# Kernel optimization log

Measured on AMD Instinct MI355X. Metric: run time of the kernel, lower is better.

## Reference

```python
import jax, jax.numpy as jnp
import numpy as np

N_NODES = 100000
N_EDGES = 1600000
N_GRAPHS = 256
D_IN = 128
D_HID = 128
D_OUT = 64


def graph_conv(x, src, dst, W_rel, b_rel, W_root):
    # PyG GraphConv: out = lin_rel(mean_{j->i} x_j) + lin_root(x)
    msgs = jax.ops.segment_sum(x[src], dst, num_segments=N_NODES)  # [N, d]
    deg = jax.ops.segment_sum(jnp.ones((src.shape[0],), x.dtype), dst, num_segments=N_NODES)
    agg = msgs / jnp.maximum(deg, 1.0)[:, None]
    return agg @ W_rel + b_rel + x @ W_root


def setup_inputs() -> dict:
    key = jax.random.key(0)
    ks = jax.random.split(key, 12)
    x = jax.random.normal(ks[0], (N_NODES, D_IN), dtype=jnp.float32)
    edge_index = jax.random.randint(ks[1], (2, N_EDGES), 0, N_NODES, dtype=jnp.int64)
    batch = jnp.sort(jax.random.randint(ks[2], (N_NODES,), 0, N_GRAPHS, dtype=jnp.int64))
    def lin(k, fan_in, fan_out):
        bound = 1.0 / np.sqrt(fan_in)
        return jax.random.uniform(k, (fan_in, fan_out), jnp.float32, -bound, bound)
    inp = {
        "x": x, "edge_index": edge_index, "batch": batch,
        "W1_rel": lin(ks[3], D_IN, D_HID), "b1_rel": jnp.zeros((D_HID,), jnp.float32), "W1_root": lin(ks[4], D_IN, D_HID),
        "W2_rel": lin(ks[5], D_HID, D_HID), "b2_rel": jnp.zeros((D_HID,), jnp.float32), "W2_root": lin(ks[6], D_HID, D_HID),
        "W3_rel": lin(ks[7], D_HID, D_HID), "b3_rel": jnp.zeros((D_HID,), jnp.float32), "W3_root": lin(ks[8], D_HID, D_HID),
        "Wl": lin(ks[9], D_HID, D_OUT), "bl": jnp.zeros((D_OUT,), jnp.float32),
    }
    return inp


def reference(x, edge_index, batch, W1_rel, b1_rel, W1_root, W2_rel, b2_rel, W2_root,
              W3_rel, b3_rel, W3_root, Wl, bl):
    src, dst = edge_index[0], edge_index[1]
    h = jax.nn.relu(graph_conv(x, src, dst, W1_rel, b1_rel, W1_root))
    h = jax.nn.relu(graph_conv(h, src, dst, W2_rel, b2_rel, W2_root))
    h = graph_conv(h, src, dst, W3_rel, b3_rel, W3_root)
    # global mean pool over graphs
    sums = jax.ops.segment_sum(h, batch, num_segments=N_GRAPHS)          # [G, d]
    cnts = jax.ops.segment_sum(jnp.ones((h.shape[0],), h.dtype), batch, num_segments=N_GRAPHS)
    pooled = sums / jnp.maximum(cnts, 1.0)[:, None]
    # dropout is identity at inference
    return pooled @ Wl + bl  # [G, D_OUT]
```

## Files before the change

### kernel.cpp

```cpp
#include <hip/hip_runtime.h>
#include <hip/hip_bf16.h>

#define N_NODES  100000
#define N_EDGES  1600000
#define N_GRAPHS 256
#define DCH      128
#define DOUT     64
#define NB       391
#define PADB     512
#define SLACK    4608
#define CHUNK    4096
#define PCH      64

typedef short v8s __attribute__((ext_vector_type(8)));
typedef float v4f __attribute__((ext_vector_type(4)));

static __device__ __forceinline__ float bf2f(unsigned short u) {
    unsigned int x = ((unsigned int)u) << 16;
    return __builtin_bit_cast(float, x);
}
static __device__ __forceinline__ unsigned short f2bf(float f) {
    unsigned int x = __builtin_bit_cast(unsigned int, f);
    unsigned int r = (x + 0x7fffu + ((x >> 16) & 1u)) >> 16;
    return (unsigned short)r;
}
static __device__ __forceinline__ int clampi(int v, int lo, int hi) {
    return v < lo ? lo : (v > hi ? hi : v);
}

__global__ void cvt_kernel(const float* __restrict__ in, unsigned short* __restrict__ out) {
    size_t i = ((size_t)blockIdx.x * blockDim.x + threadIdx.x) * 4;
    if (i + 3 < (size_t)N_NODES * DCH) {
        float4 f = *reinterpret_cast<const float4*>(in + i);
        uint2 o;
        o.x = ((unsigned)f2bf(f.y) << 16) | (unsigned)f2bf(f.x);
        o.y = ((unsigned)f2bf(f.w) << 16) | (unsigned)f2bf(f.z);
        *reinterpret_cast<uint2*>(out + i) = o;
    }
}

__global__ void __launch_bounds__(256) binA_kernel(const int* __restrict__ src, const int* __restrict__ dst,
                                                   int* __restrict__ gcur, uint2* __restrict__ region) {
    __shared__ uint2 stage[CHUNK];
    __shared__ int hcnt[PADB], hcnt2[PADB], hoff[PADB], garr[PADB];
    __shared__ int s2[256];
    int tid = threadIdx.x;
    int e0  = blockIdx.x * CHUNK;
    int nedge = N_EDGES - e0; if (nedge > CHUNK) nedge = CHUNK;

    for (int b = tid; b < PADB; b += 256) { hcnt[b] = 0; hcnt2[b] = 0; }
    __syncthreads();

    int es[16], ed[16];
    #pragma unroll
    for (int j = 0; j < 16; j++) {
        int e = e0 + j * 256 + tid;
        if (e < N_EDGES) {
            es[j] = clampi(src[e], 0, N_NODES - 1);
            ed[j] = clampi(dst[e], 0, N_NODES - 1);
            atomicAdd(&hcnt[ed[j] >> 8], 1);
        } else { es[j] = -1; ed[j] = 0; }
    }
    __syncthreads();

    int v0 = hcnt[2 * tid], v1 = hcnt[2 * tid + 1];
    s2[tid] = v0 + v1; __syncthreads();
    for (int off = 1; off < 256; off <<= 1) {
        int x = (tid >= off) ? s2[tid - off] : 0;
        __syncthreads();
        s2[tid] += x;
        __syncthreads();
    }
    int excl = s2[tid] - (v0 + v1);
    hoff[2 * tid] = excl; hoff[2 * tid + 1] = excl + v0;
    __syncthreads();

    for (int b = tid; b < NB; b += 256) {
        int c = hcnt[b];
        garr[b] = b * SLACK + ((c > 0) ? atomicAdd(&gcur[b], c) : 0);
    }
    __syncthreads();

    #pragma unroll
    for (int j = 0; j < 16; j++) {
        if (es[j] >= 0) {
            int b = ed[j] >> 8;
            int pos = atomicAdd(&hcnt2[b], 1) + hoff[b];
            stage[pos] = (uint2){(unsigned)es[j], (unsigned)ed[j]};
        }
    }
    __syncthreads();

    for (int i = tid; i < nedge; i += 256) {
        uint2 en = stage[i];
        int b = (int)(en.y >> 8);
        int gpos = garr[b] + (i - hoff[b]);
        if (gpos < (b + 1) * SLACK) region[gpos] = en;
    }
}

__global__ void __launch_bounds__(256) binFinish_kernel(const uint2* __restrict__ region, const int* __restrict__ gcur,
                                                        int* __restrict__ rowptr, int* __restrict__ csr) {
    __shared__ int h[256], sc[256], cur[256], s2[256], hoff[PADB];
    int b = blockIdx.x, tid = threadIdx.x;
    int c0 = gcur[2 * tid];     if (c0 > SLACK) c0 = SLACK;
    int c1 = gcur[2 * tid + 1]; if (c1 > SLACK) c1 = SLACK;
    s2[tid] = c0 + c1;
    h[tid] = 0;
    __syncthreads();
    for (int off = 1; off < 256; off <<= 1) {
        int x = (tid >= off) ? s2[tid - off] : 0;
        __syncthreads();
        s2[tid] += x;
        __syncthreads();
    }
    int excl = s2[tid] - (c0 + c1);
    hoff[2 * tid] = excl; hoff[2 * tid + 1] = excl + c0;
    __syncthreads();
    if (b == 0 && tid == 255) rowptr[N_NODES] = hoff[511];
    int base = hoff[b];
    int size = gcur[b]; if (size > SLACK) size = SLACK;
    int node0 = b * 256;
    for (int j = tid; j < size; j += 256) {
        unsigned loc = region[b * SLACK + j].y - (unsigned)node0;
        if (loc < 256u) atomicAdd(&h[loc], 1);
    }
    __syncthreads();
    int v = h[tid]; sc[tid] = v; __syncthreads();
    for (int off = 1; off < 256; off <<= 1) {
        int x = (tid >= off) ? sc[tid - off] : 0;
        __syncthreads();
        sc[tid] += x;
        __syncthreads();
    }
    int myptr = base + sc[tid] - v;
    int node = node0 + tid;
    if (node < N_NODES) rowptr[node] = myptr;
    cur[tid] = myptr;
    __syncthreads();
    for (int j = tid; j < size; j += 256) {
        uint2 en = region[b * SLACK + j];
        unsigned loc = en.y - (unsigned)node0;
        if (loc < 256u) {
            int p = atomicAdd(&cur[loc], 1);
            if (p >= 0 && p < N_EDGES) csr[p] = (int)en.x;
        }
    }
}

__global__ void wfrag_kernel(const float* __restrict__ W1rel, const float* __restrict__ W1root,
                             const float* __restrict__ W2rel, const float* __restrict__ W2root,
                             const float* __restrict__ W3rel, const float* __restrict__ W3root,
                             unsigned short* __restrict__ frag) {
    int gid = blockIdx.x * blockDim.x + threadIdx.x;
    if (gid >= 3 * 8 * 8 * 64) return;
    int lane = gid & 63;
    int nt   = (gid >> 6) & 7;
    int kt   = (gid >> 9) & 7;
    int L    = gid >> 12;
    const float* rel  = (L == 0) ? W1rel  : (L == 1) ? W2rel  : W3rel;
    const float* root = (L == 0) ? W1root : (L == 1) ? W2root : W3root;
    int n  = nt * 16 + (lane & 15);
    int k0 = kt * 32 + (lane >> 4) * 8;
    unsigned short o[8];
    #pragma unroll
    for (int j = 0; j < 8; j++) {
        int k = k0 + j;
        float w = (k < 128) ? rel[k * 128 + n] : root[(k - 128) * 128 + n];
        o[j] = f2bf(w);
    }
    uint4 u;
    u.x = (unsigned)o[0] | ((unsigned)o[1] << 16);
    u.y = (unsigned)o[2] | ((unsigned)o[3] << 16);
    u.z = (unsigned)o[4] | ((unsigned)o[5] << 16);
    u.w = (unsigned)o[6] | ((unsigned)o[7] << 16);
    *reinterpret_cast<uint4*>(frag + (size_t)gid * 8) = u;
}

__global__ void __launch_bounds__(64, 4) layer_kernel(
    const unsigned short* __restrict__ hin,
    const int* __restrict__ rowptr, const int* __restrict__ csr,
    const unsigned short* __restrict__ frag, const float* __restrict__ bias,
    unsigned short* __restrict__ hout, int relu)
{
    __shared__ __attribute__((aligned(16))) unsigned short As[32 * DCH];
    const int lane = threadIdx.x & 63;
    const int l16  = lane & 15;
    const int quad = lane >> 4;
    const int base = blockIdx.x * 32;

    int rp = rowptr[base + (lane < 33 ? lane : 32)];

    char* Asb = reinterpret_cast<char*>(As);

    for (int i = 0; i < 32; i++) {
        int r0 = __builtin_amdgcn_readlane(rp, i);
        int r1 = __builtin_amdgcn_readlane(rp, i + 1);
        float a0 = 0.f, a1 = 0.f;
        for (int c = r0; c < r1; c += 16) {
            int e = c + l16;
            int idx = (e < r1) ? csr[e] : N_NODES;
            #pragma unroll
            for (int j = 0; j < 16; j++) {
                int s = __builtin_amdgcn_readlane(idx, j);
                unsigned v = *reinterpret_cast<const unsigned*>(hin + (size_t)s * DCH + lane * 2);
                a0 += bf2f((unsigned short)(v & 0xffffu));
                a1 += bf2f((unsigned short)(v >> 16));
            }
        }
        int deg = r1 - r0;
        float inv = 1.0f / (float)(deg > 1 ? deg : 1);
        unsigned o = ((unsigned)f2bf(a1 * inv) << 16) | (unsigned)f2bf(a0 * inv);
        *reinterpret_cast<unsigned*>(Asb + i * 256 + ((lane * 4) ^ ((i & 7) << 4))) = o;
    }

    v4f acc[2][8];
    #pragma unroll
    for (int h = 0; h < 2; h++)
        #pragma unroll
        for (int nt = 0; nt < 8; nt++) acc[h][nt] = (v4f){0.f, 0.f, 0.f, 0.f};

    #pragma unroll
    for (int kt = 0; kt < 8; kt++) {
        v8s a0v, a1v;
        if (kt < 4) {
            int co = (kt * 64 + quad * 16) ^ ((l16 & 7) << 4);
            a0v = *reinterpret_cast<const v8s*>(Asb + l16 * 256 + co);
            a1v = *reinterpret_cast<const v8s*>(Asb + (16 + l16) * 256 + co);
        } else {
            int ak = (kt - 4) * 32 + quad * 8;
            a0v = *reinterpret_cast<const v8s*>(hin + (size_t)(base + l16) * DCH + ak);
            a1v = *reinterpret_cast<const v8s*>(hin + (size_t)(base + 16 + l16) * DCH + ak);
        }
        #pragma unroll
        for (int nt = 0; nt < 8; nt++) {
            v8s b = *reinterpret_cast<const v8s*>(frag + (((size_t)(kt * 8 + nt)) * 64 + lane) * 8);
            acc[0][nt] = __builtin_amdgcn_mfma_f32_16x16x32_bf16(a0v, b, acc[0][nt], 0, 0, 0);
            acc[1][nt] = __builtin_amdgcn_mfma_f32_16x16x32_bf16(a1v, b, acc[1][nt], 0, 0, 0);
        }
    }
    #pragma unroll
    for (int h = 0; h < 2; h++) {
        int mbase = base + h * 16 + quad * 4;
        #pragma unroll
        for (int nt = 0; nt < 8; nt++) {
            int n = nt * 16 + l16;
            float bv = bias[n];
            #pragma unroll
            for (int r = 0; r < 4; r++) {
                float v = acc[h][nt][r] + bv;
                if (relu) v = fmaxf(v, 0.f);
                hout[(size_t)(mbase + r) * DCH + n] = f2bf(v);
            }
        }
    }
}

__global__ void __launch_bounds__(128) pool_kernel(const unsigned short* __restrict__ h,
                                                   const int* __restrict__ batch,
                                                   float* __restrict__ psum) {
    int c  = threadIdx.x;
    int n0 = blockIdx.x * PCH;
    int n1 = n0 + PCH < N_NODES ? n0 + PCH : N_NODES;
    if (n0 >= n1) return;
    int cur = clampi(batch[n0], 0, N_GRAPHS - 1);
    float acc = 0.f;
    for (int n = n0; n < n1; n++) {
        int g = clampi(batch[n], 0, N_GRAPHS - 1);
        if (g != cur) {
            atomicAdd(&psum[cur * DCH + c], acc);
            acc = 0.f; cur = g;
        }
        acc += bf2f(h[(size_t)n * DCH + c]);
    }
    atomicAdd(&psum[cur * DCH + c], acc);
}

static __device__ __forceinline__ int lowerb(const int* __restrict__ a, int n, int key) {
    int lo = 0, hi = n;
    while (lo < hi) { int mid = (lo + hi) >> 1; if (a[mid] < key) lo = mid + 1; else hi = mid; }
    return lo;
}

__global__ void __launch_bounds__(64) final_kernel(const float* __restrict__ psum,
                                                   const int* __restrict__ batch,
                                                   const float* __restrict__ Wl, const float* __restrict__ bl,
                                                   float* __restrict__ out) {
    __shared__ float ps[DCH];
    __shared__ int bounds[2];
    int g = blockIdx.x, tid = threadIdx.x;
    if (tid == 0) {
        bounds[0] = lowerb(batch, N_NODES, g);
        bounds[1] = lowerb(batch, N_NODES, g + 1);
    }
    __syncthreads();
    int cnt = bounds[1] - bounds[0];
    float inv = 1.0f / (float)(cnt > 1 ? cnt : 1);
    ps[tid] = psum[g * DCH + tid] * inv;
    ps[tid + 64] = psum[g * DCH + tid + 64] * inv;
    __syncthreads();
    float o = 0.f;
    #pragma unroll 4
    for (int c = 0; c < DCH; c++) o += ps[c] * Wl[c * DOUT + tid];
    out[g * DOUT + tid] = o + bl[tid];
}

extern "C" void kernel_launch(void* const* d_in, const int* in_sizes, int n_in,
                              void* d_out, int out_size, void* d_ws, size_t ws_size,
                              hipStream_t stream) {
    const float* x     = (const float*)d_in[0];
    const int*   edge  = (const int*)d_in[1];
    const int*   src   = edge;
    const int*   dst   = edge + N_EDGES;
    const int*   batch = (const int*)d_in[2];
    const float* W1rel  = (const float*)d_in[3];
    const float* b1     = (const float*)d_in[4];
    const float* W1root = (const float*)d_in[5];
    const float* W2rel  = (const float*)d_in[6];
    const float* b2     = (const float*)d_in[7];
    const float* W2root = (const float*)d_in[8];
    const float* W3rel  = (const float*)d_in[9];
    const float* b3     = (const float*)d_in[10];
    const float* W3root = (const float*)d_in[11];
    const float* Wl     = (const float*)d_in[12];
    const float* bl     = (const float*)d_in[13];
    float* out = (float*)d_out;

    char* ws = (char*)d_ws;
    size_t off = 0;
    auto carve = [&](size_t bytes) -> void* {
        void* p = ws + off;
        off += (bytes + 255) & ~(size_t)255;
        return p;
    };
    int*            rowptr  = (int*)carve((size_t)(N_NODES + 1) * 4);
    int*            csr     = (int*)carve((size_t)(N_EDGES + 16) * 4);
    int*            gcur    = (int*)carve((size_t)PADB * 4 + (size_t)N_GRAPHS * DCH * 4);
    float*          psum    = (float*)(gcur + PADB);
    unsigned short* frag    = (unsigned short*)carve((size_t)3 * 8 * 8 * 64 * 8 * 2);
    unsigned short* B1      = (unsigned short*)carve((size_t)(N_NODES + 1) * DCH * 2);
    unsigned short* B2      = (unsigned short*)carve((size_t)(N_NODES + 1) * DCH * 2);
    uint2*          region  = (uint2*)B1;

    hipMemsetAsync(gcur, 0, (size_t)PADB * 4 + (size_t)N_GRAPHS * DCH * 4, stream);
    hipMemsetAsync(B1 + (size_t)N_NODES * DCH, 0, (size_t)DCH * 2, stream);
    hipMemsetAsync(B2 + (size_t)N_NODES * DCH, 0, (size_t)DCH * 2, stream);

    binA_kernel<<<(N_EDGES + CHUNK - 1) / CHUNK, 256, 0, stream>>>(src, dst, gcur, region);
    binFinish_kernel<<<NB, 256, 0, stream>>>(region, gcur, rowptr, csr);
    cvt_kernel<<<(N_NODES * DCH / 4 + 255) / 256, 256, 0, stream>>>(x, B2);
    wfrag_kernel<<<(3 * 8 * 8 * 64 + 255) / 256, 256, 0, stream>>>(W1rel, W1root, W2rel, W2root, W3rel, W3root, frag);

    const int layerGrid = N_NODES / 32;

    layer_kernel<<<layerGrid, 64, 0, stream>>>(B2, rowptr, csr, frag,         b1, B1, 1);
    layer_kernel<<<layerGrid, 64, 0, stream>>>(B1, rowptr, csr, frag + 32768, b2, B2, 1);
    layer_kernel<<<layerGrid, 64, 0, stream>>>(B2, rowptr, csr, frag + 65536, b3, B1, 0);

    pool_kernel<<<(N_NODES + PCH - 1) / PCH, 128, 0, stream>>>(B1, batch, psum);
    final_kernel<<<N_GRAPHS, 64, 0, stream>>>(psum, batch, Wl, bl, out);
}
```

Measured before the change: 423.8 us.

## Flatten per-node gather into a contiguous edge stream with prefetched indices

The layer kernel's aggregation now walks the whole edge range of its 32 nodes as one flat stream in groups of 16. It prefetches the next group's CSR indices and issues all 16 row loads before accumulating, flushing a node's mean whenever an edge index crosses its row boundary. This removes the per-node tail waste and the serialised load-then-add pattern for low-degree nodes. Blocks now hold two waves of 32 nodes each. The bin prefix scan is moved into a separate single-block kernel so each binFinish block no longer redoes it, and the binning chunk and pool chunk sizes are halved. The risk is more branchy control flow in the flush loop and extra register pressure from holding 16 loaded values.

After: 414.9 us. 2.1% less time.

```diff
diff --git a/kernel.cpp b/kernel.cpp
--- a/kernel.cpp
+++ b/kernel.cpp
@@ -9,8 +9,8 @@
 #define NB       391
 #define PADB     512
 #define SLACK    4608
-#define CHUNK    4096
-#define PCH      64
+#define CHUNK    2048
+#define PCH      32
 
 typedef short v8s __attribute__((ext_vector_type(8)));
 typedef float v4f __attribute__((ext_vector_type(4)));
@@ -51,9 +51,9 @@
     for (int b = tid; b < PADB; b += 256) { hcnt[b] = 0; hcnt2[b] = 0; }
     __syncthreads();
 
-    int es[16], ed[16];
-    #pragma unroll
-    for (int j = 0; j < 16; j++) {
+    int es[CHUNK / 256], ed[CHUNK / 256];
+    #pragma unroll
+    for (int j = 0; j < CHUNK / 256; j++) {
         int e = e0 + j * 256 + tid;
         if (e < N_EDGES) {
             es[j] = clampi(src[e], 0, N_NODES - 1);
@@ -82,7 +82,7 @@
     __syncthreads();
 
     #pragma unroll
-    for (int j = 0; j < 16; j++) {
+    for (int j = 0; j < CHUNK / 256; j++) {
         if (es[j] >= 0) {
             int b = ed[j] >> 8;
             int pos = atomicAdd(&hcnt2[b], 1) + hoff[b];
@@ -99,15 +99,13 @@
     }
 }
 
-__global__ void __launch_bounds__(256) binFinish_kernel(const uint2* __restrict__ region, const int* __restrict__ gcur,
-                                                        int* __restrict__ rowptr, int* __restrict__ csr) {
-    __shared__ int h[256], sc[256], cur[256], s2[256], hoff[PADB];
-    int b = blockIdx.x, tid = threadIdx.x;
+__global__ void __launch_bounds__(256) scan_kernel(const int* __restrict__ gcur,
+                                                   int* __restrict__ hoffG, int* __restrict__ rowptr) {
+    __shared__ int s2[256];
+    int tid = threadIdx.x;
     int c0 = gcur[2 * tid];     if (c0 > SLACK) c0 = SLACK;
     int c1 = gcur[2 * tid + 1]; if (c1 > SLACK) c1 = SLACK;
-    s2[tid] = c0 + c1;
-    h[tid] = 0;
-    __syncthreads();
+    s2[tid] = c0 + c1; __syncthreads();
     for (int off = 1; off < 256; off <<= 1) {
         int x = (tid >= off) ? s2[tid - off] : 0;
         __syncthreads();
@@ -115,12 +113,20 @@
         __syncthreads();
     }
     int excl = s2[tid] - (c0 + c1);
-    hoff[2 * tid] = excl; hoff[2 * tid + 1] = excl + c0;
-    __syncthreads();
-    if (b == 0 && tid == 255) rowptr[N_NODES] = hoff[511];
-    int base = hoff[b];
+    hoffG[2 * tid] = excl; hoffG[2 * tid + 1] = excl + c0;
+    if (tid == 255) rowptr[N_NODES] = s2[255];
+}
+
+__global__ void __launch_bounds__(256) binFinish_kernel(const uint2* __restrict__ region, const int* __restrict__ gcur,
+                                                        const int* __restrict__ hoffG,
+                                                        int* __restrict__ rowptr, int* __restrict__ csr) {
+    __shared__ int h[256], sc[256], cur[256];
+    int b = blockIdx.x, tid = threadIdx.x;
+    h[tid] = 0;
+    int base = hoffG[b];
     int size = gcur[b]; if (size > SLACK) size = SLACK;
     int node0 = b * 256;
+    __syncthreads();
     for (int j = tid; j < size; j += 256) {
         unsigned loc = region[b * SLACK + j].y - (unsigned)node0;
         if (loc < 256u) atomicAdd(&h[loc], 1);
@@ -177,41 +183,73 @@
     *reinterpret_cast<uint4*>(frag + (size_t)gid * 8) = u;
 }
 
-__global__ void __launch_bounds__(64, 4) layer_kernel(
+__global__ void __launch_bounds__(128, 4) layer_kernel(
     const unsigned short* __restrict__ hin,
     const int* __restrict__ rowptr, const int* __restrict__ csr,
     const unsigned short* __restrict__ frag, const float* __restrict__ bias,
     unsigned short* __restrict__ hout, int relu)
 {
-    __shared__ __attribute__((aligned(16))) unsigned short As[32 * DCH];
+    __shared__ __attribute__((aligned(16))) unsigned short As[2][32 * DCH];
+    const int wave = threadIdx.x >> 6;
     const int lane = threadIdx.x & 63;
     const int l16  = lane & 15;
     const int quad = lane >> 4;
-    const int base = blockIdx.x * 32;
+    const int base = blockIdx.x * 64 + wave * 32;
+    if (base >= N_NODES) return;
+
+    char* Asb = reinterpret_cast<char*>(As[wave]);
 
     int rp = rowptr[base + (lane < 33 ? lane : 32)];
-
-    char* Asb = reinterpret_cast<char*>(As);
-
-    for (int i = 0; i < 32; i++) {
-        int r0 = __builtin_amdgcn_readlane(rp, i);
-        int r1 = __builtin_amdgcn_readlane(rp, i + 1);
-        float a0 = 0.f, a1 = 0.f;
-        for (int c = r0; c < r1; c += 16) {
-            int e = c + l16;
-            int idx = (e < r1) ? csr[e] : N_NODES;
-            #pragma unroll
-            for (int j = 0; j < 16; j++) {
-                int s = __builtin_amdgcn_readlane(idx, j);
-                unsigned v = *reinterpret_cast<const unsigned*>(hin + (size_t)s * DCH + lane * 2);
-                a0 += bf2f((unsigned short)(v & 0xffffu));
-                a1 += bf2f((unsigned short)(v >> 16));
+    const int R0 = __builtin_amdgcn_readlane(rp, 0);
+    const int R1 = __builtin_amdgcn_readlane(rp, 32);
+
+    int ni     = 0;
+    int nstart = R0;
+    int nend   = __builtin_amdgcn_readlane(rp, 1);
+    float a0 = 0.f, a1 = 0.f;
+
+    int t0  = csr[R0 + l16];
+    int idx = (R0 + l16 < R1) ? t0 : N_NODES;
+
+    for (int e0 = R0; e0 < R1; e0 += 16) {
+        int en   = e0 + 16 + l16;
+        int tn   = csr[en];
+        int idxn = (en < R1) ? tn : N_NODES;
+
+        unsigned v[16];
+        #pragma unroll
+        for (int j = 0; j < 16; j++) {
+            int s = __builtin_amdgcn_readlane(idx, j);
+            v[j] = *reinterpret_cast<const unsigned*>(hin + (size_t)s * DCH + lane * 2);
+        }
+
+        #pragma unroll
+        for (int j = 0; j < 16; j++) {
+            int e = e0 + j;
+            while (ni < 32 && e == nend) {
+                int deg = nend - nstart;
+                float inv = 1.0f / (float)(deg > 1 ? deg : 1);
+                unsigned o = ((unsigned)f2bf(a1 * inv) << 16) | (unsigned)f2bf(a0 * inv);
+                *reinterpret_cast<unsigned*>(Asb + ni * 256 + ((lane * 4) ^ ((ni & 7) << 4))) = o;
+                a0 = 0.f; a1 = 0.f;
+                ni++;
+                nstart = nend;
+                nend = __builtin_amdgcn_readlane(rp, ni + 1);
             }
-        }
-        int deg = r1 - r0;
+            a0 += bf2f((unsigned short)(v[j] & 0xffffu));
+            a1 += bf2f((unsigned short)(v[j] >> 16));
+        }
+        idx = idxn;
+    }
+    while (ni < 32) {
+        int deg = nend - nstart;
         float inv = 1.0f / (float)(deg > 1 ? deg : 1);
         unsigned o = ((unsigned)f2bf(a1 * inv) << 16) | (unsigned)f2bf(a0 * inv);
-        *reinterpret_cast<unsigned*>(Asb + i * 256 + ((lane * 4) ^ ((i & 7) << 4))) = o;
+        *reinterpret_cast<unsigned*>(Asb + ni * 256 + ((lane * 4) ^ ((ni & 7) << 4))) = o;
+        a0 = 0.f; a1 = 0.f;
+        ni++;
+        nstart = nend;
+        nend = __builtin_amdgcn_readlane(rp, ni + 1 < 33 ? ni + 1 : 32);
     }
 
     v4f acc[2][8];
@@ -334,9 +372,10 @@
         return p;
     };
     int*            rowptr  = (int*)carve((size_t)(N_NODES + 1) * 4);
-    int*            csr     = (int*)carve((size_t)(N_EDGES + 16) * 4);
+    int*            csr     = (int*)carve((size_t)(N_EDGES + 64) * 4);
     int*            gcur    = (int*)carve((size_t)PADB * 4 + (size_t)N_GRAPHS * DCH * 4);
     float*          psum    = (float*)(gcur + PADB);
+    int*            hoffG   = (int*)carve((size_t)PADB * 4);
     unsigned short* frag    = (unsigned short*)carve((size_t)3 * 8 * 8 * 64 * 8 * 2);
     unsigned short* B1      = (unsigned short*)carve((size_t)(N_NODES + 1) * DCH * 2);
     unsigned short* B2      = (unsigned short*)carve((size_t)(N_NODES + 1) * DCH * 2);
@@ -347,15 +386,16 @@
     hipMemsetAsync(B2 + (size_t)N_NODES * DCH, 0, (size_t)DCH * 2, stream);
 
     binA_kernel<<<(N_EDGES + CHUNK - 1) / CHUNK, 256, 0, stream>>>(src, dst, gcur, region);
-    binFinish_kernel<<<NB, 256, 0, stream>>>(region, gcur, rowptr, csr);
+    scan_kernel<<<1, 256, 0, stream>>>(gcur, hoffG, rowptr);
+    binFinish_kernel<<<NB, 256, 0, stream>>>(region, gcur, hoffG, rowptr, csr);
     cvt_kernel<<<(N_NODES * DCH / 4 + 255) / 256, 256, 0, stream>>>(x, B2);
     wfrag_kernel<<<(3 * 8 * 8 * 64 + 255) / 256, 256, 0, stream>>>(W1rel, W1root, W2rel, W2root, W3rel, W3root, frag);
 
-    const int layerGrid = N_NODES / 32;
-
-    layer_kernel<<<layerGrid, 64, 0, stream>>>(B2, rowptr, csr, frag,         b1, B1, 1);
-    layer_kernel<<<layerGrid, 64, 0, stream>>>(B1, rowptr, csr, frag + 32768, b2, B2, 1);
-    layer_kernel<<<layerGrid, 64, 0, stream>>>(B2, rowptr, csr, frag + 65536, b3, B1, 0);
+    const int layerGrid = (N_NODES + 63) / 64;
+
+    layer_kernel<<<layerGrid, 128, 0, stream>>>(B2, rowptr, csr, frag,         b1, B1, 1);
+    layer_kernel<<<layerGrid, 128, 0, stream>>>(B1, rowptr, csr, frag + 32768, b2, B2, 1);
+    layer_kernel<<<layerGrid, 128, 0, stream>>>(B2, rowptr, csr, frag + 65536, b3, B1, 0);
 
     pool_kernel<<<(N_NODES + PCH - 1) / PCH, 128, 0, stream>>>(B1, batch, psum);
     final_kernel<<<N_GRAPHS, 64, 0, stream>>>(psum, batch, Wl, bl, out);
```
